# Optimization experiments

Hardware: AMD Instinct MI355X
Metric: run time of the kernel (lower is better)

The kernel has to match this reference:

```python
import jax, jax.numpy as jnp
import numpy as np

N = 50000
E = 1600000
IN_DIM = 128
HID = 64


def setup_inputs() -> dict:
    key = jax.random.key(0)
    ks = jax.random.split(key, 8)
    x = jax.random.normal(ks[0], (N, IN_DIM), dtype=jnp.float32)
    edge_row = jax.random.randint(ks[1], (E,), 0, N, dtype=jnp.int32)
    edge_col = jax.random.randint(ks[2], (E,), 0, N, dtype=jnp.int32)
    edge_val = jax.random.uniform(ks[3], (E,), dtype=jnp.float32)
    W1 = jax.random.normal(ks[4], (IN_DIM, HID), dtype=jnp.float32) * (1.0 / np.sqrt(IN_DIM))
    b1 = jnp.zeros((HID,), dtype=jnp.float32)
    W2 = jax.random.normal(ks[5], (HID, 1), dtype=jnp.float32) * (1.0 / np.sqrt(HID))
    b2 = jnp.zeros((1,), dtype=jnp.float32)
    return {"x": x, "edge_row": edge_row, "edge_col": edge_col,
            "edge_val": edge_val, "W1": W1, "b1": b1, "W2": W2, "b2": b2}


def reference(x, edge_row, edge_col, edge_val, W1, b1, W2, b2):
    # h = tanh(x @ W1 + b1)  -> [N, HID]
    h = jnp.tanh(x @ W1 + b1)
    # sparse adjacency matmul: out[i] = sum_{e: row[e]==i} val[e] * h[col[e]]
    gathered = edge_val[:, None] * h[edge_col]            # [E, HID]
    agg = jax.ops.segment_sum(gathered, edge_row, num_segments=N)  # [N, HID]
    # final linear projection to scalar per node
    return agg @ W2 + b2                                   # [N, 1]
```

## Files before the change

### kernel.cpp

```cpp
#include <hip/hip_runtime.h>
#include <hip/hip_bf16.h>

#define IN_DIM 128
#define HID 64
#define SHIFT 7
#define RPB 128
#define NBPAD 512
#define CAP 6144
#define SBLK 256
#define LDK 136

typedef __attribute__((ext_vector_type(8))) short bf16x8;
typedef __attribute__((ext_vector_type(4))) float f32x4;

__device__ __forceinline__ unsigned short f2bf(float f) {
    __hip_bfloat16 h = __float2bfloat16(f);
    return *reinterpret_cast<unsigned short*>(&h);
}

__global__ __launch_bounds__(256) void node_kernel(
    const float* __restrict__ x, const float* __restrict__ W1,
    const float* __restrict__ b1, const float* __restrict__ W2,
    float* __restrict__ g, int n, int* __restrict__ gcnt)
{
    __shared__ unsigned short sx[64 * LDK];
    __shared__ unsigned short sw[HID * LDK];
    if (blockIdx.x == 0)
        for (int i = threadIdx.x; i < NBPAD; i += 256) gcnt[i] = 0;

    const int node0 = blockIdx.x * 64;

    for (int i = threadIdx.x; i < 64 * 16; i += 256) {
        int r = i >> 4, c = i & 15;
        int gn = min(node0 + r, n - 1);
        const float4* src = reinterpret_cast<const float4*>(x + (size_t)gn * IN_DIM + c * 8);
        float4 f0 = src[0], f1 = src[1];
        union { unsigned short u[8]; uint4 v; } pk;
        pk.u[0] = f2bf(f0.x); pk.u[1] = f2bf(f0.y);
        pk.u[2] = f2bf(f0.z); pk.u[3] = f2bf(f0.w);
        pk.u[4] = f2bf(f1.x); pk.u[5] = f2bf(f1.y);
        pk.u[6] = f2bf(f1.z); pk.u[7] = f2bf(f1.w);
        *reinterpret_cast<uint4*>(&sx[r * LDK + c * 8]) = pk.v;
    }
    for (int i = threadIdx.x; i < IN_DIM * HID; i += 256) {
        int k = i >> 6, h = i & 63;
        sw[h * LDK + k] = f2bf(W1[i]);
    }

    const int wv = threadIdx.x >> 6;
    const int ln = threadIdx.x & 63;
    const int lg = ln >> 4;
    const int li = ln & 15;
    const int rowl = wv * 16 + li;
    const int kb0 = lg * 8;

    f32x4 acc[4];
    #pragma unroll
    for (int t = 0; t < 4; ++t) {
        float bj = b1[t * 16 + li];
        acc[t] = (f32x4){bj, bj, bj, bj};
    }
    __syncthreads();

    #pragma unroll
    for (int ks = 0; ks < 4; ++ks) {
        bf16x8 af = *reinterpret_cast<const bf16x8*>(&sx[rowl * LDK + ks * 32 + kb0]);
        #pragma unroll
        for (int t = 0; t < 4; ++t) {
            bf16x8 bfv = *reinterpret_cast<const bf16x8*>(&sw[(t * 16 + li) * LDK + ks * 32 + kb0]);
            acc[t] = __builtin_amdgcn_mfma_f32_16x16x32_bf16(af, bfv, acc[t], 0, 0, 0);
        }
    }

    float s[4] = {0.f, 0.f, 0.f, 0.f};
    #pragma unroll
    for (int t = 0; t < 4; ++t) {
        float w2 = W2[t * 16 + li];
        #pragma unroll
        for (int r = 0; r < 4; ++r) {
            float a = fminf(fmaxf(acc[t][r], -15.f), 15.f);
            float ex = __expf(2.f * a);
            s[r] += ((ex - 1.f) / (ex + 1.f)) * w2;
        }
    }
    #pragma unroll
    for (int off = 1; off < 16; off <<= 1) {
        #pragma unroll
        for (int r = 0; r < 4; ++r) s[r] += __shfl_xor(s[r], off);
    }
    if (li == 0) {
        #pragma unroll
        for (int r = 0; r < 4; ++r) {
            int nd = node0 + wv * 16 + lg * 4 + r;
            if (nd < n) g[nd] = s[r];
        }
    }
}

__global__ __launch_bounds__(1024) void scatter_kernel(
    const int* __restrict__ erow, const int* __restrict__ ecol,
    const float* __restrict__ ev, int e, int chunk,
    int* __restrict__ gcnt, uint2* __restrict__ pairs)
{
    __shared__ int h[NBPAD];
    __shared__ int cur[NBPAD];
    for (int i = threadIdx.x; i < NBPAD; i += 1024) h[i] = 0;
    __syncthreads();
    const int s = blockIdx.x * chunk, t = min(e, s + chunk);
    const int cnt = t - s, cnt4 = cnt >> 2;

    const int4*   r4 = reinterpret_cast<const int4*>(erow + s);
    const int4*   c4 = reinterpret_cast<const int4*>(ecol + s);
    const float4* v4 = reinterpret_cast<const float4*>(ev + s);

    for (int i = threadIdx.x; i < cnt4; i += 1024) {
        int4 r = r4[i];
        atomicAdd(&h[r.x >> SHIFT], 1);
        atomicAdd(&h[r.y >> SHIFT], 1);
        atomicAdd(&h[r.z >> SHIFT], 1);
        atomicAdd(&h[r.w >> SHIFT], 1);
    }
    for (int i = s + (cnt4 << 2) + threadIdx.x; i < t; i += 1024)
        atomicAdd(&h[erow[i] >> SHIFT], 1);
    __syncthreads();
    for (int b = threadIdx.x; b < NBPAD; b += 1024)
        cur[b] = h[b] ? atomicAdd(&gcnt[b], h[b]) : 0;
    __syncthreads();

    for (int i = threadIdx.x; i < cnt4; i += 1024) {
        int4 r = r4[i]; int4 c = c4[i]; float4 v = v4[i];
        {
            int b = r.x >> SHIFT; int pos = atomicAdd(&cur[b], 1);
            if (pos < CAP) pairs[(size_t)b * CAP + pos] =
                make_uint2(((unsigned)(r.x & (RPB-1)) << 16) | (unsigned)c.x, __float_as_uint(v.x));
        }
        {
            int b = r.y >> SHIFT; int pos = atomicAdd(&cur[b], 1);
            if (pos < CAP) pairs[(size_t)b * CAP + pos] =
                make_uint2(((unsigned)(r.y & (RPB-1)) << 16) | (unsigned)c.y, __float_as_uint(v.y));
        }
        {
            int b = r.z >> SHIFT; int pos = atomicAdd(&cur[b], 1);
            if (pos < CAP) pairs[(size_t)b * CAP + pos] =
                make_uint2(((unsigned)(r.z & (RPB-1)) << 16) | (unsigned)c.z, __float_as_uint(v.z));
        }
        {
            int b = r.w >> SHIFT; int pos = atomicAdd(&cur[b], 1);
            if (pos < CAP) pairs[(size_t)b * CAP + pos] =
                make_uint2(((unsigned)(r.w & (RPB-1)) << 16) | (unsigned)c.w, __float_as_uint(v.w));
        }
    }
    for (int i = s + (cnt4 << 2) + threadIdx.x; i < t; i += 1024) {
        int r = erow[i];
        int b = r >> SHIFT; int pos = atomicAdd(&cur[b], 1);
        if (pos < CAP) pairs[(size_t)b * CAP + pos] =
            make_uint2(((unsigned)(r & (RPB-1)) << 16) | (unsigned)ecol[i], __float_as_uint(ev[i]));
    }
}

__global__ __launch_bounds__(1024) void reduce_kernel(
    const uint2* __restrict__ pairs, const int* __restrict__ gcnt,
    const float* __restrict__ g, const float* __restrict__ b2,
    float* __restrict__ out, int n)
{
    __shared__ float acc[RPB];
    const int b = blockIdx.x;
    if (threadIdx.x < RPB) acc[threadIdx.x] = 0.f;
    __syncthreads();
    const int m = min(gcnt[b], CAP);
    const uint2* p = pairs + (size_t)b * CAP;

    int i = threadIdx.x;
    for (; i + 3072 < m; i += 4096) {
        uint2 e0 = p[i], e1 = p[i + 1024], e2 = p[i + 2048], e3 = p[i + 3072];
        float g0 = g[e0.x & 0xFFFF], g1 = g[e1.x & 0xFFFF];
        float g2 = g[e2.x & 0xFFFF], g3 = g[e3.x & 0xFFFF];
        atomicAdd(&acc[e0.x >> 16], __uint_as_float(e0.y) * g0);
        atomicAdd(&acc[e1.x >> 16], __uint_as_float(e1.y) * g1);
        atomicAdd(&acc[e2.x >> 16], __uint_as_float(e2.y) * g2);
        atomicAdd(&acc[e3.x >> 16], __uint_as_float(e3.y) * g3);
    }
    for (; i < m; i += 1024) {
        uint2 eu = p[i];
        atomicAdd(&acc[eu.x >> 16], __uint_as_float(eu.y) * g[eu.x & 0xFFFF]);
    }
    __syncthreads();
    if (threadIdx.x < RPB) {
        int r = (b << SHIFT) + threadIdx.x;
        if (r < n) out[r] = acc[threadIdx.x] + b2[0];
    }
}

extern "C" void kernel_launch(void* const* d_in, const int* in_sizes, int n_in,
                              void* d_out, int out_size, void* d_ws, size_t ws_size,
                              hipStream_t stream) {
    const float* x    = (const float*)d_in[0];
    const int*   erow = (const int*)  d_in[1];
    const int*   ecol = (const int*)  d_in[2];
    const float* ev   = (const float*)d_in[3];
    const float* W1   = (const float*)d_in[4];
    const float* b1   = (const float*)d_in[5];
    const float* W2   = (const float*)d_in[6];
    const float* b2   = (const float*)d_in[7];
    float* out = (float*)d_out;

    const int n  = in_sizes[0] / IN_DIM;
    const int e  = in_sizes[1];
    const int nb = (n + RPB - 1) >> SHIFT;

    char* ws = (char*)d_ws;
    float* g = (float*)ws;
    size_t off = ((size_t)n * 4 + 255) & ~(size_t)255;
    int* gcnt = (int*)(ws + off); off += NBPAD * 4;
    uint2* pairs = (uint2*)(ws + off);

    const int chunk = (((e + SBLK - 1) / SBLK) + 3) & ~3;

    node_kernel   <<<(n + 63) / 64, 256, 0, stream>>>(x, W1, b1, W2, g, n, gcnt);
    scatter_kernel<<<SBLK, 1024, 0, stream>>>(erow, ecol, ev, e, chunk, gcnt, pairs);
    reduce_kernel <<<nb, 1024, 0, stream>>>(pairs, gcnt, g, b2, out, n);
}
```

Baseline: 131.1 us.

## Stage scatter records in LDS by bucket before coalesced global write

```diff
diff --git a/kernel.cpp b/kernel.cpp
--- a/kernel.cpp
+++ b/kernel.cpp
@@ -8,6 +8,7 @@
 #define NBPAD 512
 #define CAP 6144
 #define SBLK 256
+#define CHUNK_MAX 6400
 #define LDK 136
 
 typedef __attribute__((ext_vector_type(8))) short bf16x8;
@@ -102,59 +103,77 @@
     const float* __restrict__ ev, int e, int chunk,
     int* __restrict__ gcnt, uint2* __restrict__ pairs)
 {
-    __shared__ int h[NBPAD];
-    __shared__ int cur[NBPAD];
-    for (int i = threadIdx.x; i < NBPAD; i += 1024) h[i] = 0;
-    __syncthreads();
+    __shared__ uint2 rec[CHUNK_MAX];
+    __shared__ int h[NBPAD], lbase[NBPAD], lcur[NBPAD], gB[NBPAD];
+    __shared__ int scanA[NBPAD], scanB[NBPAD];
+
+    const int tid = threadIdx.x;
+    for (int i = tid; i < NBPAD; i += 1024) h[i] = 0;
+    __syncthreads();
+
     const int s = blockIdx.x * chunk, t = min(e, s + chunk);
-    const int cnt = t - s, cnt4 = cnt >> 2;
+    const int cnt = t - s, cnt4 = cnt > 0 ? (cnt >> 2) : 0;
 
     const int4*   r4 = reinterpret_cast<const int4*>(erow + s);
     const int4*   c4 = reinterpret_cast<const int4*>(ecol + s);
     const float4* v4 = reinterpret_cast<const float4*>(ev + s);
 
-    for (int i = threadIdx.x; i < cnt4; i += 1024) {
+    for (int i = tid; i < cnt4; i += 1024) {
         int4 r = r4[i];
         atomicAdd(&h[r.x >> SHIFT], 1);
         atomicAdd(&h[r.y >> SHIFT], 1);
         atomicAdd(&h[r.z >> SHIFT], 1);
         atomicAdd(&h[r.w >> SHIFT], 1);
     }
-    for (int i = s + (cnt4 << 2) + threadIdx.x; i < t; i += 1024)
-        atomicAdd(&h[erow[i] >> SHIFT], 1);
-    __syncthreads();
-    for (int b = threadIdx.x; b < NBPAD; b += 1024)
-        cur[b] = h[b] ? atomicAdd(&gcnt[b], h[b]) : 0;
-    __syncthreads();
-
-    for (int i = threadIdx.x; i < cnt4; i += 1024) {
+    for (int i = (cnt4 << 2) + tid; i < cnt; i += 1024)
+        atomicAdd(&h[erow[s + i] >> SHIFT], 1);
+    __syncthreads();
+
+    int* src = scanA; int* dst = scanB;
+    if (tid < NBPAD) src[tid] = h[tid];
+    __syncthreads();
+    for (int off = 1; off < NBPAD; off <<= 1) {
+        if (tid < NBPAD) dst[tid] = src[tid] + (tid >= off ? src[tid - off] : 0);
+        __syncthreads();
+        int* tmp = src; src = dst; dst = tmp;
+    }
+    if (tid < NBPAD) {
+        int lb = tid ? src[tid - 1] : 0;
+        lbase[tid] = lb;
+        lcur[tid]  = lb;
+        gB[tid] = h[tid] ? atomicAdd(&gcnt[tid], h[tid]) : 0;
+    }
+    __syncthreads();
+
+    for (int i = tid; i < cnt4; i += 1024) {
         int4 r = r4[i]; int4 c = c4[i]; float4 v = v4[i];
-        {
-            int b = r.x >> SHIFT; int pos = atomicAdd(&cur[b], 1);
-            if (pos < CAP) pairs[(size_t)b * CAP + pos] =
-                make_uint2(((unsigned)(r.x & (RPB-1)) << 16) | (unsigned)c.x, __float_as_uint(v.x));
-        }
-        {
-            int b = r.y >> SHIFT; int pos = atomicAdd(&cur[b], 1);
-            if (pos < CAP) pairs[(size_t)b * CAP + pos] =
-                make_uint2(((unsigned)(r.y & (RPB-1)) << 16) | (unsigned)c.y, __float_as_uint(v.y));
-        }
-        {
-            int b = r.z >> SHIFT; int pos = atomicAdd(&cur[b], 1);
-            if (pos < CAP) pairs[(size_t)b * CAP + pos] =
-                make_uint2(((unsigned)(r.z & (RPB-1)) << 16) | (unsigned)c.z, __float_as_uint(v.z));
-        }
-        {
-            int b = r.w >> SHIFT; int pos = atomicAdd(&cur[b], 1);
-            if (pos < CAP) pairs[(size_t)b * CAP + pos] =
-                make_uint2(((unsigned)(r.w & (RPB-1)) << 16) | (unsigned)c.w, __float_as_uint(v.w));
-        }
-    }
-    for (int i = s + (cnt4 << 2) + threadIdx.x; i < t; i += 1024) {
-        int r = erow[i];
-        int b = r >> SHIFT; int pos = atomicAdd(&cur[b], 1);
-        if (pos < CAP) pairs[(size_t)b * CAP + pos] =
-            make_uint2(((unsigned)(r & (RPB-1)) << 16) | (unsigned)ecol[i], __float_as_uint(ev[i]));
+        int p0 = atomicAdd(&lcur[r.x >> SHIFT], 1);
+        rec[p0] = make_uint2(((unsigned)(r.x & (RPB-1)) << 16) | (unsigned)c.x, __float_as_uint(v.x));
+        int p1 = atomicAdd(&lcur[r.y >> SHIFT], 1);
+        rec[p1] = make_uint2(((unsigned)(r.y & (RPB-1)) << 16) | (unsigned)c.y, __float_as_uint(v.y));
+        int p2 = atomicAdd(&lcur[r.z >> SHIFT], 1);
+        rec[p2] = make_uint2(((unsigned)(r.z & (RPB-1)) << 16) | (unsigned)c.z, __float_as_uint(v.z));
+        int p3 = atomicAdd(&lcur[r.w >> SHIFT], 1);
+        rec[p3] = make_uint2(((unsigned)(r.w & (RPB-1)) << 16) | (unsigned)c.w, __float_as_uint(v.w));
+    }
+    for (int i = (cnt4 << 2) + tid; i < cnt; i += 1024) {
+        int r = erow[s + i];
+        int p = atomicAdd(&lcur[r >> SHIFT], 1);
+        rec[p] = make_uint2(((unsigned)(r & (RPB-1)) << 16) | (unsigned)ecol[s + i],
+                            __float_as_uint(ev[s + i]));
+    }
+    __syncthreads();
+
+    const int wv = tid >> 6, ln = tid & 63;
+    for (int b = wv; b < NBPAD; b += 16) {
+        const int hb = h[b];
+        if (!hb) continue;
+        const int lb = lbase[b], gb = gB[b];
+        uint2* dstp = pairs + (size_t)b * CAP;
+        for (int j = ln; j < hb; j += 64) {
+            int gpos = gb + j;
+            if (gpos < CAP) dstp[gpos] = rec[lb + j];
+        }
     }
 }
 
```

After: 126.6 us. 3.4% less time.
